# Performance work log

Hardware: AMD Instinct MI355X
Metric: run time of the kernel (lower is better)

Reference implementation:

```python
import jax, jax.numpy as jnp
import numpy as np

N_NODES = 20000
N_EDGES = 240000
IN_DIM = 20
SH_DIM = 16  # (lmax+1)^2 with lmax=3
DENOM = 1.0
EPS = 1e-12


def spherical_harmonics_lmax3(v):
    """Real spherical harmonics l=0..3 on unit vectors v: [E,3] -> [E,16]."""
    x, y, z = v[:, 0], v[:, 1], v[:, 2]
    x2, y2, z2 = x * x, y * y, z * z
    sh = [
        jnp.full_like(x, 0.28209479177387814),            # l=0
        0.4886025119029199 * y,                            # l=1, m=-1
        0.4886025119029199 * z,                            # l=1, m=0
        0.4886025119029199 * x,                            # l=1, m=1
        1.0925484305920792 * x * y,                        # l=2, m=-2
        1.0925484305920792 * y * z,                        # l=2, m=-1
        0.31539156525252005 * (3.0 * z2 - 1.0),            # l=2, m=0
        1.0925484305920792 * x * z,                        # l=2, m=1
        0.5462742152960396 * (x2 - y2),                    # l=2, m=2
        0.5900435899266435 * y * (3.0 * x2 - y2),          # l=3, m=-3
        2.890611442640554 * x * y * z,                     # l=3, m=-2
        0.4570457994644658 * y * (5.0 * z2 - 1.0),         # l=3, m=-1
        0.3731763325901154 * z * (5.0 * z2 - 3.0),         # l=3, m=0
        0.4570457994644658 * x * (5.0 * z2 - 1.0),         # l=3, m=1
        1.445305721320277 * z * (x2 - y2),                 # l=3, m=2
        0.5900435899266435 * x * (x2 - 3.0 * y2),          # l=3, m=3
    ]
    return jnp.stack(sh, axis=-1)


def setup_inputs() -> dict:
    key = jax.random.key(0)
    ks = jax.random.split(key, 10)
    x = jax.random.normal(ks[0], (N_NODES, IN_DIM), dtype=jnp.float32)
    positions = jax.random.normal(ks[1], (N_NODES, 3), dtype=jnp.float32)
    edge_index = jax.random.randint(ks[2], (2, N_EDGES), 0, N_NODES, dtype=jnp.int32)
    s = 1.0 / np.sqrt(IN_DIM)
    W_pre = jax.random.uniform(ks[3], (IN_DIM, IN_DIM), jnp.float32, -s, s)
    b_pre = jax.random.uniform(ks[4], (IN_DIM,), jnp.float32, -s, s)
    W_post = jax.random.uniform(ks[5], (IN_DIM, IN_DIM), jnp.float32, -s, s)
    b_post = jax.random.uniform(ks[6], (IN_DIM,), jnp.float32, -s, s)
    W_sc = jax.random.uniform(ks[7], (IN_DIM, IN_DIM), jnp.float32, -s, s)
    b_sc = jax.random.uniform(ks[8], (IN_DIM,), jnp.float32, -s, s)
    return {"x": x, "positions": positions, "edge_index": edge_index,
            "W_pre": W_pre, "b_pre": b_pre, "W_post": W_post, "b_post": b_post,
            "W_sc": W_sc, "b_sc": b_sc}


def reference(x, positions, edge_index, W_pre, b_pre, W_post, b_post, W_sc, b_sc):
    row, col = edge_index[0], edge_index[1]
    # per-edge gather + relative positions
    rel = positions[col] - positions[row]                      # [E,3]
    norm = jnp.sqrt(jnp.sum(rel * rel, axis=-1, keepdims=True) + EPS)
    sh = spherical_harmonics_lmax3(rel / norm)                 # [E,16]
    sender = x[row]                                            # [E,20]
    # equivariant tensor product (outer product over irreps channels)
    tp = (sender[:, :, None] * sh[:, None, :]).reshape(sender.shape[0], IN_DIM * SH_DIM)  # [E,320]
    edge_features = jnp.concatenate([sender, tp], axis=1)      # [E,340]
    # scatter-add aggregation to target nodes
    aggr = jax.ops.segment_sum(edge_features, col, num_segments=N_NODES)  # [N,340]
    # node update MLP + shortcut (math of Layer.update)
    h = x / DENOM
    h = jax.nn.relu(h @ W_pre.T + b_pre)
    h = h @ W_post.T + b_post
    out = x @ W_sc.T + b_sc + h                                # [N,20]
    # aggr is computed (and aggregated) by the original propagate; concat so it stays live
    return jnp.concatenate([out, aggr], axis=1)                # [N,360]
```

## Files before the change

### kernel.cpp

```cpp
#include <hip/hip_runtime.h>
#include <stdint.h>

#define N_NODES 20000
#define N_EDGES 240000
#define IN_DIM  20
#define OUT_DIM 360
#define EPS_F   1e-12f
#define NPART   8
#define CAP_P   16
#define SLOTS   (NPART * CAP_P)
#define EDGE_BLOCKS ((N_EDGES + 255) / 256)
#define MLP_BLOCKS  ((N_NODES + 255) / 256)

typedef _Float16 half8   __attribute__((ext_vector_type(8)));
typedef float    floatx16 __attribute__((ext_vector_type(16)));

__device__ __forceinline__ half8 h8_from_u32(uint32_t u0, uint32_t u1,
                                             uint32_t u2, uint32_t u3) {
    union { uint32_t u[4]; half8 h; } t;
    t.u[0] = u0; t.u[1] = u1; t.u[2] = u2; t.u[3] = u3;
    return t.h;
}

__device__ __forceinline__ uint32_t maskpair(int t, int j) {
    return (t > j ? 0xFFFFu : 0u) | (t > j + 1 ? 0xFFFF0000u : 0u);
}

__device__ __forceinline__ float sh_coeff(int k, float xn, float yn, float zn) {
    const float x2 = xn * xn, y2 = yn * yn, z2 = zn * zn;
    switch (k) {
        case 0:  return 0.28209479177387814f;
        case 1:  return 0.4886025119029199f * yn;
        case 2:  return 0.4886025119029199f * zn;
        case 3:  return 0.4886025119029199f * xn;
        case 4:  return 1.0925484305920792f * xn * yn;
        case 5:  return 1.0925484305920792f * yn * zn;
        case 6:  return 0.31539156525252005f * (3.0f * z2 - 1.0f);
        case 7:  return 1.0925484305920792f * xn * zn;
        case 8:  return 0.5462742152960396f * (x2 - y2);
        case 9:  return 0.5900435899266435f * yn * (3.0f * x2 - y2);
        case 10: return 2.890611442640554f  * xn * yn * zn;
        case 11: return 0.4570457994644658f * yn * (5.0f * z2 - 1.0f);
        case 12: return 0.3731763325901154f * zn * (5.0f * z2 - 3.0f);
        case 13: return 0.4570457994644658f * xn * (5.0f * z2 - 1.0f);
        case 14: return 1.445305721320277f  * zn * (x2 - y2);
        default: return 0.5900435899266435f * xn * (x2 - 3.0f * y2);
    }
}

__global__ __launch_bounds__(256) void bucket_sh_mlp(
    const float* __restrict__ pos,
    const int* __restrict__ ei,
    const float* __restrict__ x,
    const float* __restrict__ Wpre,  const float* __restrict__ bpre,
    const float* __restrict__ Wpost, const float* __restrict__ bpost,
    const float* __restrict__ Wsc,   const float* __restrict__ bsc,
    int* __restrict__ cnt_pad,
    int* __restrict__ ovf_cnt,
    int* __restrict__ ovf,
    int* __restrict__ bucket,
    half8* __restrict__ shbuf,
    uint32_t* __restrict__ xpair,
    float* __restrict__ out)
{
    if ((int)blockIdx.x < EDGE_BLOCKS) {
        const int e = (int)(blockIdx.x * 256 + threadIdx.x);
        if (e >= N_EDGES) return;
        const int p = (int)(blockIdx.x & (NPART - 1));
        const int row = ei[e];
        const int col = ei[N_EDGES + e];
        const int slot = atomicAdd(&cnt_pad[((size_t)(p * N_NODES + col)) << 4], 1);
        if (slot >= CAP_P) { ovf[atomicAdd(ovf_cnt, 1)] = e; return; }

        const int sidx = col * SLOTS + (p << 4) + slot;
        bucket[sidx] = row;

        const float rx = pos[col * 3 + 0] - pos[row * 3 + 0];
        const float ry = pos[col * 3 + 1] - pos[row * 3 + 1];
        const float rz = pos[col * 3 + 2] - pos[row * 3 + 2];
        const float rinv = rsqrtf(rx * rx + ry * ry + rz * rz + EPS_F);
        const float xx = rx * rinv, yy = ry * rinv, zz = rz * rinv;
        const float x2 = xx * xx, y2 = yy * yy, z2 = zz * zz;

        const float sh0  = 0.28209479177387814f;
        const float sh1  = 0.4886025119029199f * yy;
        const float sh2  = 0.4886025119029199f * zz;
        const float sh3  = 0.4886025119029199f * xx;
        const float sh4  = 1.0925484305920792f * xx * yy;
        const float sh5  = 1.0925484305920792f * yy * zz;
        const float sh6  = 0.31539156525252005f * (3.0f * z2 - 1.0f);
        const float sh7  = 1.0925484305920792f * xx * zz;
        const float sh8  = 0.5462742152960396f * (x2 - y2);
        const float sh9  = 0.5900435899266435f * yy * (3.0f * x2 - y2);
        const float sh10 = 2.890611442640554f  * xx * yy * zz;
        const float sh11 = 0.4570457994644658f * yy * (5.0f * z2 - 1.0f);
        const float sh12 = 0.3731763325901154f * zz * (5.0f * z2 - 3.0f);
        const float sh13 = 0.4570457994644658f * xx * (5.0f * z2 - 1.0f);
        const float sh14 = 1.445305721320277f  * zz * (x2 - y2);
        const float sh15 = 0.5900435899266435f * xx * (x2 - 3.0f * y2);

        const half8 v0 = { (_Float16)sh0,  (_Float16)sh1,  (_Float16)sh2,  (_Float16)sh3,
                           (_Float16)sh4,  (_Float16)sh5,  (_Float16)sh6,  (_Float16)sh7 };
        const half8 v1 = { (_Float16)sh8,  (_Float16)sh9,  (_Float16)sh10, (_Float16)sh11,
                           (_Float16)sh12, (_Float16)sh13, (_Float16)sh14, (_Float16)sh15 };
        half8* dst = shbuf + (size_t)sidx * 2;
        dst[0] = v0;
        dst[1] = v1;
        return;
    }

    __shared__ float sWpre[IN_DIM * IN_DIM];
    __shared__ float sWpost[IN_DIM * IN_DIM];
    __shared__ float sWsc[IN_DIM * IN_DIM];
    __shared__ float sb[3 * IN_DIM];

    for (int t = threadIdx.x; t < IN_DIM * IN_DIM; t += 256) {
        sWpre[t]  = Wpre[t];
        sWpost[t] = Wpost[t];
        sWsc[t]   = Wsc[t];
    }
    if (threadIdx.x < IN_DIM) {
        sb[threadIdx.x]              = bpre[threadIdx.x];
        sb[IN_DIM + threadIdx.x]     = bpost[threadIdx.x];
        sb[2 * IN_DIM + threadIdx.x] = bsc[threadIdx.x];
    }
    __syncthreads();

    const int i = (int)((blockIdx.x - EDGE_BLOCKS) * 256 + threadIdx.x);
    if (i >= N_NODES) return;

    float xi[IN_DIM], h[IN_DIM];
#pragma unroll
    for (int j = 0; j < IN_DIM; ++j) xi[j] = x[(size_t)i * IN_DIM + j];

#pragma unroll
    for (int j = 0; j < IN_DIM; ++j) {
        const float v = xi[j];
        const _Float16 hh = (_Float16)v;
        const float res = v - (float)hh;
        union { _Float16 f[2]; uint32_t u; } t;
        t.f[0] = hh; t.f[1] = (_Float16)res;
        xpair[(size_t)i * IN_DIM + j] = t.u;
    }

#pragma unroll
    for (int j = 0; j < IN_DIM; ++j) {
        float a = sb[j];
#pragma unroll
        for (int kk = 0; kk < IN_DIM; ++kk) a = fmaf(xi[kk], sWpre[j * IN_DIM + kk], a);
        h[j] = fmaxf(a, 0.0f);
    }
#pragma unroll
    for (int j = 0; j < IN_DIM; ++j) {
        float a = sb[IN_DIM + j] + sb[2 * IN_DIM + j];
#pragma unroll
        for (int kk = 0; kk < IN_DIM; ++kk) {
            a = fmaf(h[kk],  sWpost[j * IN_DIM + kk], a);
            a = fmaf(xi[kk], sWsc[j * IN_DIM + kk],  a);
        }
        out[(size_t)i * OUT_DIM + j] = a;
    }
}

__global__ __launch_bounds__(256) void node_gather(
    const float* __restrict__ x,
    const float* __restrict__ pos,
    const int* __restrict__ ei,
    const int* __restrict__ cnt_pad,
    const int* __restrict__ bucket,
    const _Float16* __restrict__ shbuf,
    const uint32_t* __restrict__ xpair,
    const int* __restrict__ ovf_cnt,
    const int* __restrict__ ovf,
    float* __restrict__ out)
{
    const int lane  = threadIdx.x & 63;
    const int node  = (int)((blockIdx.x * blockDim.x + threadIdx.x) >> 6);
    const int col   = lane & 31;
    const int hi    = lane >> 5;
    const int khalf = hi * 8;
    const int rowc  = min(col, IN_DIM - 1);

    int ovf_any = 0;
    int c[NPART];
#pragma unroll
    for (int q = 0; q < NPART; ++q) {
        const int cr = __builtin_amdgcn_readfirstlane(
            cnt_pad[((size_t)(q * N_NODES + node)) << 4]);
        ovf_any |= (cr > CAP_P);
        c[q] = min(cr, CAP_P);
    }
    int pre = 0, pp = 0, base = 0;
#pragma unroll
    for (int q = 0; q < NPART; ++q) {
        if (q >= 1) {
            const int ge = (lane >= pre) ? 1 : 0;
            pp  += ge;
            base = ge ? pre : base;
        }
        pre += c[q];
    }
    const int cnt = min(pre, 64);
    const int s  = min(lane - base, CAP_P - 1);
    const int m  = (pp << 4) + s;

    floatx16 acc = {0,0,0,0,0,0,0,0,0,0,0,0,0,0,0,0};

    if (cnt > 0) {
        int rl = bucket[node * SLOTS + m];
        const uint16_t* sh16 = (const uint16_t*)shbuf;
        const int nb = (cnt + 15) >> 4;

        for (int b = 0; b < nb; ++b) {
            const int sbase = 16 * b + khalf;

            int rr[8];
#pragma unroll
            for (int j = 0; j < 8; ++j) {
                int r = __shfl(rl, sbase + j, 64);
                rr[j] = (int)min((uint32_t)r, (uint32_t)(N_NODES - 1));
            }
            uint32_t ee[8];
#pragma unroll
            for (int j = 0; j < 8; ++j)
                ee[j] = xpair[(size_t)rr[j] * IN_DIM + rowc];

            uint32_t hh[8];
#pragma unroll
            for (int j = 0; j < 8; ++j) {
                const int mj = __shfl(m, sbase + j, 64);
                hh[j] = sh16[(size_t)(node * SLOTS + mj) * 16 + (col & 15)];
            }

            uint32_t a1u[4], a2u[4];
#pragma unroll
            for (int pq = 0; pq < 4; ++pq) {
                a1u[pq] = (ee[2 * pq] & 0xFFFFu)  | (ee[2 * pq + 1] << 16);
                a2u[pq] = (ee[2 * pq] >> 16)      | (ee[2 * pq + 1] & 0xFFFF0000u);
            }

            uint32_t B0, B1, B2, B3;
            if (col < 16) {
                B0 = hh[0] | (hh[1] << 16);
                B1 = hh[2] | (hh[3] << 16);
                B2 = hh[4] | (hh[5] << 16);
                B3 = hh[6] | (hh[7] << 16);
            } else if (col == 16) {
                B0 = B1 = B2 = B3 = 0x3C003C00u;
            } else {
                B0 = B1 = B2 = B3 = 0u;
            }
            const int rem = cnt - 16 * b;
            if (rem < 16) {
                const int t = rem - khalf;
                B0 &= maskpair(t, 0);
                B1 &= maskpair(t, 2);
                B2 &= maskpair(t, 4);
                B3 &= maskpair(t, 6);
            }

            const half8 hb  = h8_from_u32(B0, B1, B2, B3);
            const half8 ha1 = h8_from_u32(a1u[0], a1u[1], a1u[2], a1u[3]);
            const half8 ha2 = h8_from_u32(a2u[0], a2u[1], a2u[2], a2u[3]);
            acc = __builtin_amdgcn_mfma_f32_32x32x16_f16(ha1, hb, acc, 0, 0, 0);
            acc = __builtin_amdgcn_mfma_f32_32x32x16_f16(ha2, hb, acc, 0, 0, 0);
        }
    }

    if (ovf_any) {
        const int mm = *ovf_cnt;
        for (int t2 = 0; t2 < mm; ++t2) {
            const int e = ovf[t2];
            if (ei[N_EDGES + e] != node) continue;
            const int row = ei[e];
            const float rx = pos[node * 3 + 0] - pos[row * 3 + 0];
            const float ry = pos[node * 3 + 1] - pos[row * 3 + 1];
            const float rz = pos[node * 3 + 2] - pos[row * 3 + 2];
            const float rinv = rsqrtf(rx * rx + ry * ry + rz * rz + EPS_F);
            float shc;
            if (col < 16)       shc = sh_coeff(col, rx * rinv, ry * rinv, rz * rinv);
            else if (col == 16) shc = 1.0f;
            else                shc = 0.0f;
#pragma unroll
            for (int r = 0; r < 16; ++r) {
                const int rw = ((r & 3) + 8 * (r >> 2)) + 4 * hi;
                if (rw < IN_DIM)
                    acc[r] = fmaf(x[(size_t)row * IN_DIM + rw], shc, acc[r]);
            }
        }
    }

    float* orow = out + (size_t)node * OUT_DIM;
    if (col < 16) {
#pragma unroll
        for (int r = 0; r < 16; ++r) {
            const int rw = ((r & 3) + 8 * (r >> 2)) + 4 * hi;
            if (rw < IN_DIM) orow[2 * IN_DIM + rw * 16 + col] = acc[r];
        }
    } else if (col == 16) {
#pragma unroll
        for (int r = 0; r < 16; ++r) {
            const int rw = ((r & 3) + 8 * (r >> 2)) + 4 * hi;
            if (rw < IN_DIM) orow[IN_DIM + rw] = acc[r];
        }
    }
}

extern "C" void kernel_launch(void* const* d_in, const int* in_sizes, int n_in,
                              void* d_out, int out_size, void* d_ws, size_t ws_size,
                              hipStream_t stream)
{
    const float* x     = (const float*)d_in[0];
    const float* pos   = (const float*)d_in[1];
    const int*   ei    = (const int*)d_in[2];
    const float* Wpre  = (const float*)d_in[3];
    const float* bpre  = (const float*)d_in[4];
    const float* Wpost = (const float*)d_in[5];
    const float* bpost = (const float*)d_in[6];
    const float* Wsc   = (const float*)d_in[7];
    const float* bsc   = (const float*)d_in[8];
    float* out = (float*)d_out;

    char* wp = (char*)d_ws;
    half8*    shbuf   = (half8*)wp;               wp += (size_t)N_NODES * SLOTS * 32;
    int*      bucket  = (int*)wp;                 wp += (size_t)N_NODES * SLOTS * 4;
    uint32_t* xpair   = (uint32_t*)wp;            wp += (size_t)N_NODES * IN_DIM * 4;
    int*      cnt_pad = (int*)wp;                 wp += (size_t)NPART * N_NODES * 64;
    int*      ovf_cnt = (int*)wp;                 wp += 4;
    int*      ovf     = (int*)wp;

    hipMemsetAsync(cnt_pad, 0, (size_t)NPART * N_NODES * 64 + 4, stream);

    bucket_sh_mlp<<<EDGE_BLOCKS + MLP_BLOCKS, 256, 0, stream>>>(
        pos, ei, x, Wpre, bpre, Wpost, bpost, Wsc, bsc,
        cnt_pad, ovf_cnt, ovf, bucket, shbuf, xpair, out);

    node_gather<<<(N_NODES * 64) / 256, 256, 0, stream>>>(
        x, pos, ei, cnt_pad, bucket, (const _Float16*)shbuf, xpair, ovf_cnt, ovf, out);
}
```

Baseline: 121.4 us.

## Compute spherical harmonics in gather kernel via LDS instead of global buffer

The spherical harmonics were computed per edge in the bucketing kernel and written to a large global fp16 buffer (32 bytes per slot), then read back in the gather kernel. Now each lane in the gather wavefront computes the harmonics for its bucketed edge, stores them in shared memory, and the MFMA B operand is built from LDS. This removes the global sh buffer write and read traffic but moves position gathers and rsqrt math into the gather kernel and adds a block barrier. It caps the per-node in-wave slots at 64 as before.

```diff
diff --git a/kernel.cpp b/kernel.cpp
--- a/kernel.cpp
+++ b/kernel.cpp
@@ -48,8 +48,7 @@
     }
 }
 
-__global__ __launch_bounds__(256) void bucket_sh_mlp(
-    const float* __restrict__ pos,
+__global__ __launch_bounds__(256) void bucket_mlp(
     const int* __restrict__ ei,
     const float* __restrict__ x,
     const float* __restrict__ Wpre,  const float* __restrict__ bpre,
@@ -59,7 +58,6 @@
     int* __restrict__ ovf_cnt,
     int* __restrict__ ovf,
     int* __restrict__ bucket,
-    half8* __restrict__ shbuf,
     uint32_t* __restrict__ xpair,
     float* __restrict__ out)
 {
@@ -71,13 +69,118 @@
         const int col = ei[N_EDGES + e];
         const int slot = atomicAdd(&cnt_pad[((size_t)(p * N_NODES + col)) << 4], 1);
         if (slot >= CAP_P) { ovf[atomicAdd(ovf_cnt, 1)] = e; return; }
-
-        const int sidx = col * SLOTS + (p << 4) + slot;
-        bucket[sidx] = row;
-
-        const float rx = pos[col * 3 + 0] - pos[row * 3 + 0];
-        const float ry = pos[col * 3 + 1] - pos[row * 3 + 1];
-        const float rz = pos[col * 3 + 2] - pos[row * 3 + 2];
+        bucket[col * SLOTS + (p << 4) + slot] = row;
+        return;
+    }
+
+    __shared__ float sWpre[IN_DIM * IN_DIM];
+    __shared__ float sWpost[IN_DIM * IN_DIM];
+    __shared__ float sWsc[IN_DIM * IN_DIM];
+    __shared__ float sb[3 * IN_DIM];
+
+    for (int t = threadIdx.x; t < IN_DIM * IN_DIM; t += 256) {
+        sWpre[t]  = Wpre[t];
+        sWpost[t] = Wpost[t];
+        sWsc[t]   = Wsc[t];
+    }
+    if (threadIdx.x < IN_DIM) {
+        sb[threadIdx.x]              = bpre[threadIdx.x];
+        sb[IN_DIM + threadIdx.x]     = bpost[threadIdx.x];
+        sb[2 * IN_DIM + threadIdx.x] = bsc[threadIdx.x];
+    }
+    __syncthreads();
+
+    const int i = (int)((blockIdx.x - EDGE_BLOCKS) * 256 + threadIdx.x);
+    if (i >= N_NODES) return;
+
+    float xi[IN_DIM], h[IN_DIM];
+#pragma unroll
+    for (int j = 0; j < IN_DIM; ++j) xi[j] = x[(size_t)i * IN_DIM + j];
+
+#pragma unroll
+    for (int j = 0; j < IN_DIM; ++j) {
+        const float v = xi[j];
+        const _Float16 hh = (_Float16)v;
+        const float res = v - (float)hh;
+        union { _Float16 f[2]; uint32_t u; } t;
+        t.f[0] = hh; t.f[1] = (_Float16)res;
+        xpair[(size_t)i * IN_DIM + j] = t.u;
+    }
+
+#pragma unroll
+    for (int j = 0; j < IN_DIM; ++j) {
+        float a = sb[j];
+#pragma unroll
+        for (int kk = 0; kk < IN_DIM; ++kk) a = fmaf(xi[kk], sWpre[j * IN_DIM + kk], a);
+        h[j] = fmaxf(a, 0.0f);
+    }
+#pragma unroll
+    for (int j = 0; j < IN_DIM; ++j) {
+        float a = sb[IN_DIM + j] + sb[2 * IN_DIM + j];
+#pragma unroll
+        for (int kk = 0; kk < IN_DIM; ++kk) {
+            a = fmaf(h[kk],  sWpost[j * IN_DIM + kk], a);
+            a = fmaf(xi[kk], sWsc[j * IN_DIM + kk],  a);
+        }
+        out[(size_t)i * OUT_DIM + j] = a;
+    }
+}
+
+__global__ __launch_bounds__(256) void node_gather(
+    const float* __restrict__ x,
+    const float* __restrict__ pos,
+    const int* __restrict__ ei,
+    const int* __restrict__ cnt_pad,
+    const int* __restrict__ bucket,
+    const uint32_t* __restrict__ xpair,
+    const int* __restrict__ ovf_cnt,
+    const int* __restrict__ ovf,
+    float* __restrict__ out)
+{
+    __shared__ uint16_t shls[4][64][16];
+
+    const int lane  = threadIdx.x & 63;
+    const int w     = (int)(threadIdx.x >> 6);
+    const int node  = __builtin_amdgcn_readfirstlane(
+        (int)((blockIdx.x * blockDim.x + threadIdx.x) >> 6));
+    const int col   = lane & 31;
+    const int hi    = lane >> 5;
+    const int khalf = hi * 8;
+    const int rowc  = min(col, IN_DIM - 1);
+
+    int ovf_any = 0;
+    int c[NPART];
+#pragma unroll
+    for (int q = 0; q < NPART; ++q) {
+        const int cr = __builtin_amdgcn_readfirstlane(
+            cnt_pad[((size_t)(q * N_NODES + node)) << 4]);
+        ovf_any |= (cr > CAP_P);
+        c[q] = min(cr, CAP_P);
+    }
+    int pre = 0, pp = 0, base = 0;
+#pragma unroll
+    for (int q = 0; q < NPART; ++q) {
+        if (q >= 1) {
+            const int ge = (lane >= pre) ? 1 : 0;
+            pp  += ge;
+            base = ge ? pre : base;
+        }
+        pre += c[q];
+    }
+    const int cnt = min(pre, 64);
+    const int s  = min(lane - base, CAP_P - 1);
+    const int m  = (pp << 4) + s;
+
+    const int rl = (int)min((uint32_t)bucket[node * SLOTS + m],
+                            (uint32_t)(N_NODES - 1));
+
+    {
+        const float pnx = pos[node * 3 + 0];
+        const float pny = pos[node * 3 + 1];
+        const float pnz = pos[node * 3 + 2];
+        const float rx = pnx - pos[rl * 3 + 0];
+        const float ry = pny - pos[rl * 3 + 1];
+        const float rz = pnz - pos[rl * 3 + 2];
         const float rinv = rsqrtf(rx * rx + ry * ry + rz * rz + EPS_F);
         const float xx = rx * rinv, yy = ry * rinv, zz = rz * rinv;
         const float x2 = xx * xx, y2 = yy * yy, z2 = zz * zz;
@@ -103,112 +206,15 @@
                            (_Float16)sh4,  (_Float16)sh5,  (_Float16)sh6,  (_Float16)sh7 };
         const half8 v1 = { (_Float16)sh8,  (_Float16)sh9,  (_Float16)sh10, (_Float16)sh11,
                            (_Float16)sh12, (_Float16)sh13, (_Float16)sh14, (_Float16)sh15 };
-        half8* dst = shbuf + (size_t)sidx * 2;
-        dst[0] = v0;
-        dst[1] = v1;
-        return;
-    }
-
-    __shared__ float sWpre[IN_DIM * IN_DIM];
-    __shared__ float sWpost[IN_DIM * IN_DIM];
-    __shared__ float sWsc[IN_DIM * IN_DIM];
-    __shared__ float sb[3 * IN_DIM];
-
-    for (int t = threadIdx.x; t < IN_DIM * IN_DIM; t += 256) {
-        sWpre[t]  = Wpre[t];
-        sWpost[t] = Wpost[t];
-        sWsc[t]   = Wsc[t];
-    }
-    if (threadIdx.x < IN_DIM) {
-        sb[threadIdx.x]              = bpre[threadIdx.x];
-        sb[IN_DIM + threadIdx.x]     = bpost[threadIdx.x];
-        sb[2 * IN_DIM + threadIdx.x] = bsc[threadIdx.x];
+        half8* wp = (half8*)&shls[w][lane][0];
+        wp[0] = v0;
+        wp[1] = v1;
     }
     __syncthreads();
 
-    const int i = (int)((blockIdx.x - EDGE_BLOCKS) * 256 + threadIdx.x);
-    if (i >= N_NODES) return;
-
-    float xi[IN_DIM], h[IN_DIM];
-#pragma unroll
-    for (int j = 0; j < IN_DIM; ++j) xi[j] = x[(size_t)i * IN_DIM + j];
-
-#pragma unroll
-    for (int j = 0; j < IN_DIM; ++j) {
-        const float v = xi[j];
-        const _Float16 hh = (_Float16)v;
-        const float res = v - (float)hh;
-        union { _Float16 f[2]; uint32_t u; } t;
-        t.f[0] = hh; t.f[1] = (_Float16)res;
-        xpair[(size_t)i * IN_DIM + j] = t.u;
-    }
-
-#pragma unroll
-    for (int j = 0; j < IN_DIM; ++j) {
-        float a = sb[j];
-#pragma unroll
-        for (int kk = 0; kk < IN_DIM; ++kk) a = fmaf(xi[kk], sWpre[j * IN_DIM + kk], a);
-        h[j] = fmaxf(a, 0.0f);
-    }
-#pragma unroll
-    for (int j = 0; j < IN_DIM; ++j) {
-        float a = sb[IN_DIM + j] + sb[2 * IN_DIM + j];
-#pragma unroll
-        for (int kk = 0; kk < IN_DIM; ++kk) {
-            a = fmaf(h[kk],  sWpost[j * IN_DIM + kk], a);
-            a = fmaf(xi[kk], sWsc[j * IN_DIM + kk],  a);
-        }
-        out[(size_t)i * OUT_DIM + j] = a;
-    }
-}
-
-__global__ __launch_bounds__(256) void node_gather(
-    const float* __restrict__ x,
-    const float* __restrict__ pos,
-    const int* __restrict__ ei,
-    const int* __restrict__ cnt_pad,
-    const int* __restrict__ bucket,
-    const _Float16* __restrict__ shbuf,
-    const uint32_t* __restrict__ xpair,
-    const int* __restrict__ ovf_cnt,
-    const int* __restrict__ ovf,
-    float* __restrict__ out)
-{
-    const int lane  = threadIdx.x & 63;
-    const int node  = (int)((blockIdx.x * blockDim.x + threadIdx.x) >> 6);
-    const int col   = lane & 31;
-    const int hi    = lane >> 5;
-    const int khalf = hi * 8;
-    const int rowc  = min(col, IN_DIM - 1);
-
-    int ovf_any = 0;
-    int c[NPART];
-#pragma unroll
-    for (int q = 0; q < NPART; ++q) {
-        const int cr = __builtin_amdgcn_readfirstlane(
-            cnt_pad[((size_t)(q * N_NODES + node)) << 4]);
-        ovf_any |= (cr > CAP_P);
-        c[q] = min(cr, CAP_P);
-    }
-    int pre = 0, pp = 0, base = 0;
-#pragma unroll
-    for (int q = 0; q < NPART; ++q) {
-        if (q >= 1) {
-            const int ge = (lane >= pre) ? 1 : 0;
-            pp  += ge;
-            base = ge ? pre : base;
-        }
-        pre += c[q];
-    }
-    const int cnt = min(pre, 64);
-    const int s  = min(lane - base, CAP_P - 1);
-    const int m  = (pp << 4) + s;
-
     floatx16 acc = {0,0,0,0,0,0,0,0,0,0,0,0,0,0,0,0};
 
     if (cnt > 0) {
-        int rl = bucket[node * SLOTS + m];
-        const uint16_t* sh16 = (const uint16_t*)shbuf;
         const int nb = (cnt + 15) >> 4;
 
         for (int b = 0; b < nb; ++b) {
@@ -216,35 +222,27 @@
 
             int rr[8];
 #pragma unroll
-            for (int j = 0; j < 8; ++j) {
-                int r = __shfl(rl, sbase + j, 64);
-                rr[j] = (int)min((uint32_t)r, (uint32_t)(N_NODES - 1));
-            }
+            for (int j = 0; j < 8; ++j)
+                rr[j] = __shfl(rl, sbase + j, 64);
             uint32_t ee[8];
 #pragma unroll
             for (int j = 0; j < 8; ++j)
                 ee[j] = xpair[(size_t)rr[j] * IN_DIM + rowc];
 
-            uint32_t hh[8];
-#pragma unroll
-            for (int j = 0; j < 8; ++j) {
-                const int mj = __shfl(m, sbase + j, 64);
-                hh[j] = sh16[(size_t)(node * SLOTS + mj) * 16 + (col & 15)];
-            }
-
-            uint32_t a1u[4], a2u[4];
-#pragma unroll
-            for (int pq = 0; pq < 4; ++pq) {
-                a1u[pq] = (ee[2 * pq] & 0xFFFFu)  | (ee[2 * pq + 1] << 16);
-                a2u[pq] = (ee[2 * pq] >> 16)      | (ee[2 * pq + 1] & 0xFFFF0000u);
-            }
-
             uint32_t B0, B1, B2, B3;
             if (col < 16) {
-                B0 = hh[0] | (hh[1] << 16);
-                B1 = hh[2] | (hh[3] << 16);
-                B2 = hh[4] | (hh[5] << 16);
-                B3 = hh[6] | (hh[7] << 16);
+                const uint32_t h0 = shls[w][sbase + 0][col];
+                const uint32_t h1 = shls[w][sbase + 1][col];
+                const uint32_t h2 = shls[w][sbase + 2][col];
+                const uint32_t h3 = shls[w][sbase + 3][col];
+                const uint32_t h4 = shls[w][sbase + 4][col];
+                const uint32_t h5 = shls[w][sbase + 5][col];
+                const uint32_t h6 = shls[w][sbase + 6][col];
+                const uint32_t h7 = shls[w][sbase + 7][col];
+                B0 = h0 | (h1 << 16);
+                B1 = h2 | (h3 << 16);
+                B2 = h4 | (h5 << 16);
+                B3 = h6 | (h7 << 16);
             } else if (col == 16) {
                 B0 = B1 = B2 = B3 = 0x3C003C00u;
             } else {
@@ -257,6 +255,13 @@
                 B1 &= maskpair(t, 2);
                 B2 &= maskpair(t, 4);
                 B3 &= maskpair(t, 6);
+            }
+
+            uint32_t a1u[4], a2u[4];
+#pragma unroll
+            for (int pq = 0; pq < 4; ++pq) {
+                a1u[pq] = (ee[2 * pq] & 0xFFFFu)  | (ee[2 * pq + 1] << 16);
+                a2u[pq] = (ee[2 * pq] >> 16)      | (ee[2 * pq + 1] & 0xFFFF0000u);
             }
 
             const half8 hb  = h8_from_u32(B0, B1, B2, B3);
@@ -322,7 +327,6 @@
     float* out = (float*)d_out;
 
     char* wp = (char*)d_ws;
-    half8*    shbuf   = (half8*)wp;               wp += (size_t)N_NODES * SLOTS * 32;
     int*      bucket  = (int*)wp;                 wp += (size_t)N_NODES * SLOTS * 4;
     uint32_t* xpair   = (uint32_t*)wp;            wp += (size_t)N_NODES * IN_DIM * 4;
     int*      cnt_pad = (int*)wp;                 wp += (size_t)NPART * N_NODES * 64;
@@ -331,10 +335,10 @@
 
     hipMemsetAsync(cnt_pad, 0, (size_t)NPART * N_NODES * 64 + 4, stream);
 
-    bucket_sh_mlp<<<EDGE_BLOCKS + MLP_BLOCKS, 256, 0, stream>>>(
-        pos, ei, x, Wpre, bpre, Wpost, bpost, Wsc, bsc,
-        cnt_pad, ovf_cnt, ovf, bucket, shbuf, xpair, out);
+    bucket_mlp<<<EDGE_BLOCKS + MLP_BLOCKS, 256, 0, stream>>>(
+        ei, x, Wpre, bpre, Wpost, bpost, Wsc, bsc,
+        cnt_pad, ovf_cnt, ovf, bucket, xpair, out);
 
     node_gather<<<(N_NODES * 64) / 256, 256, 0, stream>>>(
-        x, pos, ei, cnt_pad, bucket, (const _Float16*)shbuf, xpair, ovf_cnt, ovf, out);
-}
+        x, pos, ei, cnt_pad, bucket, xpair, ovf_cnt, ovf, out);
+}
```

New measurement: 116.6 us. -4.0%, faster.
